# Performance work log

Hardware: AMD Instinct MI355X
Metric: run time of the kernel (lower is better)

## Reference

```python
import jax, jax.numpy as jnp
import numpy as np

TEMPERATURE = 1.0

def setup_inputs() -> dict:
    key = jax.random.key(0)
    k1, k2 = jax.random.split(key)
    B, F, C = 16384, 2048, 1000
    features = jax.random.normal(k1, (B, F), dtype=jnp.float32)
    prototypes = jax.random.normal(k2, (C, F), dtype=jnp.float32)
    return {"features": features, "prototypes": prototypes}

def reference(features, prototypes):
    # Euclidean pairwise distance via ||a||^2 + ||b||^2 - 2 a.b (same math as cdist p=2)
    f_sq = jnp.sum(features * features, axis=-1, keepdims=True)        # [B,1]
    p_sq = jnp.sum(prototypes * prototypes, axis=-1)[None, :]          # [1,C]
    cross = jnp.einsum('bf,cf->bc', features, prototypes)              # [B,C]
    d2 = jnp.maximum(f_sq + p_sq - 2.0 * cross, 0.0)
    distances = jnp.sqrt(d2)
    logits = -distances
    return logits / TEMPERATURE
```

## Files before the change

kernel.cpp:

```cpp
#include <hip/hip_runtime.h>
#include <stdint.h>


#define KDIM 2048
#define BM 128
#define BN 128
#define BKS 32
#define NSTEPS (KDIM / BKS)

typedef __attribute__((ext_vector_type(8))) __bf16 bf16x8;
typedef __attribute__((ext_vector_type(4))) float f32x4;

__device__ __forceinline__ bool sniff_is_f32(const void* Araw) {
  const uint16_t* sniff = (const uint16_t*)Araw;
  float mx = 0.f;
#pragma unroll
  for (int i = 0; i < 64; ++i) {
    float v = __uint_as_float(((uint32_t)sniff[i]) << 16);
    mx = fmaxf(mx, fabsf(v));
  }
  return mx > 1e4f;
}

__device__ __forceinline__ uint32_t bf16rn(uint32_t u) {
  return (u + 0x7FFFu + ((u >> 16) & 1u)) >> 16;
}
__device__ __forceinline__ uint32_t pack_rn(uint32_t a, uint32_t b) {
  return bf16rn(a) | (bf16rn(b) << 16);
}

__device__ __forceinline__ void gload_lds16(const void* g, void* l) {
  __builtin_amdgcn_global_load_lds(
      (const __attribute__((address_space(1))) void*)g,
      (__attribute__((address_space(3))) void*)l, 16, 0, 0);
}

__global__ __launch_bounds__(256) void prep_kernel(
    const void* __restrict__ Araw, const void* __restrict__ Braw,
    uint16_t* __restrict__ Abf, uint16_t* __restrict__ Bbf,
    float* __restrict__ fsq, float* __restrict__ psq, int M, int N) {
  const bool isf32 = sniff_is_f32(Araw);
  const int wave = threadIdx.x >> 6;
  const int lane = threadIdx.x & 63;
  const int row = blockIdx.x * 4 + wave;
  if (row >= M + N) return;
  const bool isA = row < M;
  const size_t r = isA ? (size_t)row : (size_t)(row - M);
  uint2* dst = (uint2*)((isA ? Abf : Bbf) + r * KDIM);
  float s = 0.f;
  if (isf32) {
    const float* p = (isA ? (const float*)Araw : (const float*)Braw) + r * KDIM;
#pragma unroll
    for (int it = 0; it < KDIM / 256; ++it) {
      float4 v = *((const float4*)p + it * 64 + lane);
      s = fmaf(v.x, v.x, fmaf(v.y, v.y, fmaf(v.z, v.z, fmaf(v.w, v.w, s))));
      uint2 o;
      o.x = pack_rn(__float_as_uint(v.x), __float_as_uint(v.y));
      o.y = pack_rn(__float_as_uint(v.z), __float_as_uint(v.w));
      dst[it * 64 + lane] = o;
    }
  } else {
    const uint16_t* p =
        (isA ? (const uint16_t*)Araw : (const uint16_t*)Braw) + r * KDIM;
#pragma unroll
    for (int it = 0; it < KDIM / 256; ++it) {
      uint2 v = *((const uint2*)p + it * 64 + lane);
      float e0 = __uint_as_float(v.x << 16);
      float e1 = __uint_as_float(v.x & 0xFFFF0000u);
      float e2 = __uint_as_float(v.y << 16);
      float e3 = __uint_as_float(v.y & 0xFFFF0000u);
      s = fmaf(e0, e0, fmaf(e1, e1, fmaf(e2, e2, fmaf(e3, e3, s))));
      dst[it * 64 + lane] = v;
    }
  }
#pragma unroll
  for (int o = 32; o > 0; o >>= 1) s += __shfl_down(s, o, 64);
  if (lane == 0) {
    if (isA) fsq[r] = s;
    else     psq[r] = s;
  }
}

__global__ __launch_bounds__(256) void gemm_kernel(
    const uint16_t* __restrict__ Abf, const uint16_t* __restrict__ Bbf,
    const float* __restrict__ fsq, const float* __restrict__ psq,
    float* __restrict__ out, int M, int N) {
  __shared__ uint32_t Ab[4][BM][16];
  __shared__ uint32_t Bb[4][BN][16];

  const int tid = threadIdx.x;
  const int lane = tid & 63;
  const int wave = tid >> 6;

  const int gx = gridDim.x, gy = gridDim.y;
  const int nwg = gx * gy;
  int id = blockIdx.y * gx + blockIdx.x;
  if ((nwg & 7) == 0) id = (id & 7) * (nwg >> 3) + (id >> 3);
  const int m0 = (id / gx) * BM;
  const int n0 = (id % gx) * BN;

  const int wr = wave >> 1;
  const int wc = wave & 1;
  const int lr = lane & 15;
  const int lg = lane >> 4;

  const int wbase = (tid & ~63);

  auto stage = [&](int b, int ks) {
#pragma unroll
    for (int l = 0; l < 2; ++l) {
      const int f = l * 256 + tid;
      const int row = f >> 2;
      const int gc = (f & 3) ^ ((row >> 1) & 3);
      uint32_t* la = &Ab[b][0][0] + (l * 256 + wbase) * 4;
      uint32_t* lb = &Bb[b][0][0] + (l * 256 + wbase) * 4;
      int gm = m0 + row; gm = gm < M ? gm : M - 1;
      int gn = n0 + row; gn = gn < N ? gn : N - 1;
      gload_lds16(Abf + (size_t)gm * KDIM + ks * BKS + gc * 8, la);
      gload_lds16(Bbf + (size_t)gn * KDIM + ks * BKS + gc * 8, lb);
    }
  };

  f32x4 acc[4][4] = {};

  stage(0, 0);
  stage(1, 1);
  stage(2, 2);

  for (int ks = 0; ks < NSTEPS; ++ks) {
    const int buf = ks & 3;
    if (ks + 3 < NSTEPS) {
      stage((ks + 3) & 3, ks + 3);
      asm volatile("s_waitcnt vmcnt(12)");
    } else if (ks + 2 < NSTEPS) {
      asm volatile("s_waitcnt vmcnt(8)");
    } else if (ks + 1 < NSTEPS) {
      asm volatile("s_waitcnt vmcnt(4)");
    } else {
      asm volatile("s_waitcnt vmcnt(0)");
    }
    __builtin_amdgcn_s_barrier();
    asm volatile("" ::: "memory");

    bf16x8 ah[4], bh[4];
#pragma unroll
    for (int i = 0; i < 4; ++i) {
      const int r = wr * 64 + i * 16 + lr;
      const int pc = (lg ^ ((r >> 1) & 3)) * 4;
      ah[i] = *(const bf16x8*)&Ab[buf][r][pc];
    }
#pragma unroll
    for (int j = 0; j < 4; ++j) {
      const int r = wc * 64 + j * 16 + lr;
      const int pc = (lg ^ ((r >> 1) & 3)) * 4;
      bh[j] = *(const bf16x8*)&Bb[buf][r][pc];
    }

    __builtin_amdgcn_s_setprio(1);
#pragma unroll
    for (int i = 0; i < 4; ++i)
#pragma unroll
      for (int j = 0; j < 4; ++j)
        acc[i][j] = __builtin_amdgcn_mfma_f32_16x16x32_bf16(ah[i], bh[j],
                                                            acc[i][j], 0, 0, 0);
    __builtin_amdgcn_s_setprio(0);

    __builtin_amdgcn_s_barrier();
    asm volatile("" ::: "memory");
  }

#pragma unroll
  for (int j = 0; j < 4; ++j) {
    const int n = n0 + wc * 64 + j * 16 + lr;
    if (n >= N) continue;
    const float pn = psq[n];
#pragma unroll
    for (int i = 0; i < 4; ++i) {
      const int mb = m0 + wr * 64 + i * 16 + lg * 4;
#pragma unroll
      for (int r = 0; r < 4; ++r) {
        const int m = mb + r;
        if (m < M) {
          const float d2 = fsq[m] + pn - 2.f * acc[i][j][r];
          out[(size_t)m * N + n] = -sqrtf(fmaxf(d2, 0.f));
        }
      }
    }
  }
}

__global__ __launch_bounds__(256) void dist_mfma_kernel(
    const void* __restrict__ Araw, const void* __restrict__ Braw,
    float* __restrict__ out, int M, int N) {
  __shared__ uint32_t Ah[2][BM][16];
  __shared__ uint32_t Bh[2][BN][16];
  __shared__ float fsqs[BM];
  __shared__ float psqs[BN];

  const bool isf32 = sniff_is_f32(Araw);
  const int tid = threadIdx.x;
  const int lane = tid & 63;
  const int wave = tid >> 6;
  const int m0 = blockIdx.y * BM;
  const int n0 = blockIdx.x * BN;

  const float* A32 = (const float*)Araw;
  const float* B32 = (const float*)Braw;
  const uint16_t* A16 = (const uint16_t*)Araw;
  const uint16_t* B16 = (const uint16_t*)Braw;

  const int crow = tid >> 2;
  const int cch = tid & 3;
  const int wr = wave >> 1;
  const int wc = wave & 1;
  const int lr = lane & 15;
  const int lg = lane >> 4;

  uint4 qa0[2], qa1[2], qb0[2], qb1[2];
  float na[2] = {0.f, 0.f};
  float nb[2] = {0.f, 0.f};

  auto load_step = [&](int ks) {
#pragma unroll
    for (int s = 0; s < 2; ++s) {
      const int row = crow + 64 * s;
      int gm = m0 + row; gm = gm < M ? gm : M - 1;
      int gn = n0 + row; gn = gn < N ? gn : N - 1;
      const size_t ea = (size_t)gm * KDIM + ks * BKS + cch * 8;
      const size_t eb = (size_t)gn * KDIM + ks * BKS + cch * 8;
      if (isf32) {
        qa0[s] = *(const uint4*)(A32 + ea);
        qa1[s] = *(const uint4*)(A32 + ea + 4);
        qb0[s] = *(const uint4*)(B32 + eb);
        qb1[s] = *(const uint4*)(B32 + eb + 4);
      } else {
        qa0[s] = *(const uint4*)(A16 + ea);
        qb0[s] = *(const uint4*)(B16 + eb);
      }
    }
  };

  auto store_step = [&](int b) {
#pragma unroll
    for (int s = 0; s < 2; ++s) {
      const int row = crow + 64 * s;
      const int pc = (cch ^ ((row >> 1) & 3)) * 4;
      if (isf32) {
        const uint32_t ua[8] = {qa0[s].x, qa0[s].y, qa0[s].z, qa0[s].w,
                                qa1[s].x, qa1[s].y, qa1[s].z, qa1[s].w};
        const uint32_t ub[8] = {qb0[s].x, qb0[s].y, qb0[s].z, qb0[s].w,
                                qb1[s].x, qb1[s].y, qb1[s].z, qb1[s].w};
        float sa = 0.f, sb = 0.f;
#pragma unroll
        for (int j = 0; j < 8; ++j) {
          const float fa = __uint_as_float(ua[j]);
          const float fb = __uint_as_float(ub[j]);
          sa = fmaf(fa, fa, sa);
          sb = fmaf(fb, fb, sb);
        }
        na[s] += sa; nb[s] += sb;
        uint4 pa = {pack_rn(ua[0], ua[1]), pack_rn(ua[2], ua[3]),
                    pack_rn(ua[4], ua[5]), pack_rn(ua[6], ua[7])};
        uint4 pb = {pack_rn(ub[0], ub[1]), pack_rn(ub[2], ub[3]),
                    pack_rn(ub[4], ub[5]), pack_rn(ub[6], ub[7])};
        *(uint4*)&Ah[b][row][pc] = pa;
        *(uint4*)&Bh[b][row][pc] = pb;
      } else {
        const uint32_t va[4] = {qa0[s].x, qa0[s].y, qa0[s].z, qa0[s].w};
        const uint32_t vb[4] = {qb0[s].x, qb0[s].y, qb0[s].z, qb0[s].w};
        float sa = 0.f, sb = 0.f;
#pragma unroll
        for (int j = 0; j < 4; ++j) {
          const float a0 = __uint_as_float(va[j] << 16);
          const float a1 = __uint_as_float(va[j] & 0xFFFF0000u);
          const float b0 = __uint_as_float(vb[j] << 16);
          const float b1 = __uint_as_float(vb[j] & 0xFFFF0000u);
          sa = fmaf(a0, a0, fmaf(a1, a1, sa));
          sb = fmaf(b0, b0, fmaf(b1, b1, sb));
        }
        na[s] += sa; nb[s] += sb;
        *(uint4*)&Ah[b][row][pc] = qa0[s];
        *(uint4*)&Bh[b][row][pc] = qb0[s];
      }
    }
  };

  f32x4 acc[4][4] = {};
  load_step(0);
  store_step(0);
  __syncthreads();

  for (int ks = 0; ks < NSTEPS; ++ks) {
    const int buf = ks & 1;
    const int nxt = ks + 1;
    if (nxt < NSTEPS) load_step(nxt);

    bf16x8 ah[4], bh[4];
#pragma unroll
    for (int i = 0; i < 4; ++i) {
      const int r = wr * 64 + i * 16 + lr;
      const int pc = (lg ^ ((r >> 1) & 3)) * 4;
      ah[i] = *(const bf16x8*)&Ah[buf][r][pc];
    }
#pragma unroll
    for (int j = 0; j < 4; ++j) {
      const int r = wc * 64 + j * 16 + lr;
      const int pc = (lg ^ ((r >> 1) & 3)) * 4;
      bh[j] = *(const bf16x8*)&Bh[buf][r][pc];
    }

#pragma unroll
    for (int i = 0; i < 4; ++i)
#pragma unroll
      for (int j = 0; j < 4; ++j)
        acc[i][j] = __builtin_amdgcn_mfma_f32_16x16x32_bf16(ah[i], bh[j],
                                                            acc[i][j], 0, 0, 0);

    if (nxt < NSTEPS) store_step(nxt & 1);
    __syncthreads();
  }

  float v0 = na[0], v1 = na[1], w0 = nb[0], w1 = nb[1];
#pragma unroll
  for (int o = 1; o <= 2; o <<= 1) {
    v0 += __shfl_xor(v0, o);
    v1 += __shfl_xor(v1, o);
    w0 += __shfl_xor(w0, o);
    w1 += __shfl_xor(w1, o);
  }
  if (cch == 0) {
    fsqs[crow] = v0;
    fsqs[crow + 64] = v1;
    psqs[crow] = w0;
    psqs[crow + 64] = w1;
  }
  __syncthreads();

#pragma unroll
  for (int j = 0; j < 4; ++j) {
    const int nn = wc * 64 + j * 16 + lr;
    const int n = n0 + nn;
    if (n >= N) continue;
    const float pn = psqs[nn];
#pragma unroll
    for (int i = 0; i < 4; ++i) {
      const int mb = wr * 64 + i * 16 + lg * 4;
#pragma unroll
      for (int r = 0; r < 4; ++r) {
        const int m = m0 + mb + r;
        if (m < M) {
          const float d2 = fsqs[mb + r] + pn - 2.f * acc[i][j][r];
          out[(size_t)m * N + n] = -sqrtf(fmaxf(d2, 0.f));
        }
      }
    }
  }
}

extern "C" void kernel_launch(void* const* d_in, const int* in_sizes, int n_in,
                              void* d_out, int out_size, void* d_ws,
                              size_t ws_size, hipStream_t stream) {
  (void)n_in; (void)out_size;
  const void* feat = d_in[0];
  const void* prot = d_in[1];
  float* out = (float*)d_out;

  const int M = in_sizes[0] / KDIM;
  const int N = in_sizes[1] / KDIM;

  const size_t bfA = (size_t)M * KDIM * sizeof(uint16_t);
  const size_t bfB = (size_t)N * KDIM * sizeof(uint16_t);
  const size_t ws_need = bfA + bfB + (size_t)(M + N) * sizeof(float);

  if (d_ws != nullptr && ws_size >= ws_need) {
    uint16_t* Abf = (uint16_t*)d_ws;
    uint16_t* Bbf = (uint16_t*)((char*)d_ws + bfA);
    float* fsq = (float*)((char*)d_ws + bfA + bfB);
    float* psq = fsq + M;
    const int rows = M + N;
    prep_kernel<<<dim3((rows + 3) / 4), dim3(256), 0, stream>>>(
        feat, prot, Abf, Bbf, fsq, psq, M, N);
    dim3 grid((N + BN - 1) / BN, (M + BM - 1) / BM);
    gemm_kernel<<<grid, dim3(256), 0, stream>>>(Abf, Bbf, fsq, psq, out, M, N);
  } else {
    dim3 grid((N + BN - 1) / BN, (M + BM - 1) / BM);
    dist_mfma_kernel<<<grid, dim3(256), 0, stream>>>(feat, prot, out, M, N);
  }
}
```

Before: 344.0 us.

## Enlarge GEMM tile to 256x256x64 with 512 threads and double buffering

Result: faster. 322.0 us (-6.4%).

```diff
diff --git a/kernel.cpp b/kernel.cpp
--- a/kernel.cpp
+++ b/kernel.cpp
@@ -3,10 +3,6 @@
 
 
 #define KDIM 2048
-#define BM 128
-#define BN 128
-#define BKS 32
-#define NSTEPS (KDIM / BKS)
 
 typedef __attribute__((ext_vector_type(8))) __bf16 bf16x8;
 typedef __attribute__((ext_vector_type(4))) float f32x4;
@@ -81,12 +77,17 @@
   }
 }
 
-__global__ __launch_bounds__(256) void gemm_kernel(
+#define BM2 256
+#define BN2 256
+#define BK2 64
+#define NK2 (KDIM / BK2)
+
+__global__ __launch_bounds__(512, 2) void gemm_kernel(
     const uint16_t* __restrict__ Abf, const uint16_t* __restrict__ Bbf,
     const float* __restrict__ fsq, const float* __restrict__ psq,
     float* __restrict__ out, int M, int N) {
-  __shared__ uint32_t Ab[4][BM][16];
-  __shared__ uint32_t Bb[4][BN][16];
+  __shared__ uint32_t Ab[2][BM2][32];
+  __shared__ uint32_t Bb[2][BN2][32];
 
   const int tid = threadIdx.x;
   const int lane = tid & 63;
@@ -96,11 +97,11 @@
   const int nwg = gx * gy;
   int id = blockIdx.y * gx + blockIdx.x;
   if ((nwg & 7) == 0) id = (id & 7) * (nwg >> 3) + (id >> 3);
-  const int m0 = (id / gx) * BM;
-  const int n0 = (id % gx) * BN;
-
-  const int wr = wave >> 1;
-  const int wc = wave & 1;
+  const int m0 = (id / gx) * BM2;
+  const int n0 = (id % gx) * BN2;
+
+  const int wr = wave >> 2;
+  const int wc = wave & 3;
   const int lr = lane & 15;
   const int lg = lane >> 4;
 
@@ -108,61 +109,61 @@
 
   auto stage = [&](int b, int ks) {
 #pragma unroll
-    for (int l = 0; l < 2; ++l) {
-      const int f = l * 256 + tid;
-      const int row = f >> 2;
-      const int gc = (f & 3) ^ ((row >> 1) & 3);
-      uint32_t* la = &Ab[b][0][0] + (l * 256 + wbase) * 4;
-      uint32_t* lb = &Bb[b][0][0] + (l * 256 + wbase) * 4;
+    for (int p = 0; p < 4; ++p) {
+      const int f = p * 512 + tid;
+      const int row = f >> 3;
+      const int gc = (f & 7) ^ (row & 7);
+      uint32_t* la = &Ab[b][0][0] + (p * 512 + wbase) * 4;
+      uint32_t* lb = &Bb[b][0][0] + (p * 512 + wbase) * 4;
       int gm = m0 + row; gm = gm < M ? gm : M - 1;
       int gn = n0 + row; gn = gn < N ? gn : N - 1;
-      gload_lds16(Abf + (size_t)gm * KDIM + ks * BKS + gc * 8, la);
-      gload_lds16(Bbf + (size_t)gn * KDIM + ks * BKS + gc * 8, lb);
+      gload_lds16(Abf + (size_t)gm * KDIM + ks * BK2 + gc * 8, la);
+      gload_lds16(Bbf + (size_t)gn * KDIM + ks * BK2 + gc * 8, lb);
     }
   };
 
-  f32x4 acc[4][4] = {};
+  f32x4 acc[8][4] = {};
 
   stage(0, 0);
-  stage(1, 1);
-  stage(2, 2);
-
-  for (int ks = 0; ks < NSTEPS; ++ks) {
-    const int buf = ks & 3;
-    if (ks + 3 < NSTEPS) {
-      stage((ks + 3) & 3, ks + 3);
-      asm volatile("s_waitcnt vmcnt(12)");
-    } else if (ks + 2 < NSTEPS) {
+
+  for (int ks = 0; ks < NK2; ++ks) {
+    const int buf = ks & 1;
+    if (ks + 1 < NK2) {
+      stage(buf ^ 1, ks + 1);
       asm volatile("s_waitcnt vmcnt(8)");
-    } else if (ks + 1 < NSTEPS) {
-      asm volatile("s_waitcnt vmcnt(4)");
     } else {
       asm volatile("s_waitcnt vmcnt(0)");
     }
     __builtin_amdgcn_s_barrier();
     asm volatile("" ::: "memory");
 
-    bf16x8 ah[4], bh[4];
-#pragma unroll
-    for (int i = 0; i < 4; ++i) {
-      const int r = wr * 64 + i * 16 + lr;
-      const int pc = (lg ^ ((r >> 1) & 3)) * 4;
-      ah[i] = *(const bf16x8*)&Ab[buf][r][pc];
-    }
-#pragma unroll
-    for (int j = 0; j < 4; ++j) {
-      const int r = wc * 64 + j * 16 + lr;
-      const int pc = (lg ^ ((r >> 1) & 3)) * 4;
-      bh[j] = *(const bf16x8*)&Bb[buf][r][pc];
+    bf16x8 bh[4][2];
+#pragma unroll
+    for (int nj = 0; nj < 4; ++nj) {
+      const int r = wc * 64 + nj * 16 + lr;
+#pragma unroll
+      for (int kk = 0; kk < 2; ++kk) {
+        const int pc = ((kk * 4 + lg) ^ (r & 7)) * 4;
+        bh[nj][kk] = *(const bf16x8*)&Bb[buf][r][pc];
+      }
     }
 
     __builtin_amdgcn_s_setprio(1);
 #pragma unroll
-    for (int i = 0; i < 4; ++i)
-#pragma unroll
-      for (int j = 0; j < 4; ++j)
-        acc[i][j] = __builtin_amdgcn_mfma_f32_16x16x32_bf16(ah[i], bh[j],
-                                                            acc[i][j], 0, 0, 0);
+    for (int mi = 0; mi < 8; ++mi) {
+      const int r = wr * 128 + mi * 16 + lr;
+      const int p0 = ((0 + lg) ^ (r & 7)) * 4;
+      const int p1 = ((4 + lg) ^ (r & 7)) * 4;
+      const bf16x8 a0 = *(const bf16x8*)&Ab[buf][r][p0];
+      const bf16x8 a1 = *(const bf16x8*)&Ab[buf][r][p1];
+#pragma unroll
+      for (int nj = 0; nj < 4; ++nj) {
+        acc[mi][nj] = __builtin_amdgcn_mfma_f32_16x16x32_bf16(
+            a0, bh[nj][0], acc[mi][nj], 0, 0, 0);
+        acc[mi][nj] = __builtin_amdgcn_mfma_f32_16x16x32_bf16(
+            a1, bh[nj][1], acc[mi][nj], 0, 0, 0);
+      }
+    }
     __builtin_amdgcn_s_setprio(0);
 
     __builtin_amdgcn_s_barrier();
@@ -170,24 +171,29 @@
   }
 
 #pragma unroll
-  for (int j = 0; j < 4; ++j) {
-    const int n = n0 + wc * 64 + j * 16 + lr;
+  for (int nj = 0; nj < 4; ++nj) {
+    const int n = n0 + wc * 64 + nj * 16 + lr;
     if (n >= N) continue;
     const float pn = psq[n];
 #pragma unroll
-    for (int i = 0; i < 4; ++i) {
-      const int mb = m0 + wr * 64 + i * 16 + lg * 4;
+    for (int mi = 0; mi < 8; ++mi) {
+      const int mb = m0 + wr * 128 + mi * 16 + lg * 4;
 #pragma unroll
       for (int r = 0; r < 4; ++r) {
         const int m = mb + r;
         if (m < M) {
-          const float d2 = fsq[m] + pn - 2.f * acc[i][j][r];
+          const float d2 = fsq[m] + pn - 2.f * acc[mi][nj][r];
           out[(size_t)m * N + n] = -sqrtf(fmaxf(d2, 0.f));
         }
       }
     }
   }
 }
+
+#define BM 128
+#define BN 128
+#define BKS 32
+#define NSTEPS (KDIM / BKS)
 
 __global__ __launch_bounds__(256) void dist_mfma_kernel(
     const void* __restrict__ Araw, const void* __restrict__ Braw,
@@ -266,9 +272,9 @@
         *(uint4*)&Ah[b][row][pc] = pa;
         *(uint4*)&Bh[b][row][pc] = pb;
       } else {
+        float sa = 0.f, sb = 0.f;
         const uint32_t va[4] = {qa0[s].x, qa0[s].y, qa0[s].z, qa0[s].w};
         const uint32_t vb[4] = {qb0[s].x, qb0[s].y, qb0[s].z, qb0[s].w};
-        float sa = 0.f, sb = 0.f;
 #pragma unroll
         for (int j = 0; j < 4; ++j) {
           const float a0 = __uint_as_float(va[j] << 16);
@@ -380,8 +386,8 @@
     const int rows = M + N;
     prep_kernel<<<dim3((rows + 3) / 4), dim3(256), 0, stream>>>(
         feat, prot, Abf, Bbf, fsq, psq, M, N);
-    dim3 grid((N + BN - 1) / BN, (M + BM - 1) / BM);
-    gemm_kernel<<<grid, dim3(256), 0, stream>>>(Abf, Bbf, fsq, psq, out, M, N);
+    dim3 grid((N + BN2 - 1) / BN2, (M + BM2 - 1) / BM2);
+    gemm_kernel<<<grid, dim3(512), 0, stream>>>(Abf, Bbf, fsq, psq, out, M, N);
   } else {
     dim3 grid((N + BN - 1) / BN, (M + BM - 1) / BM);
     dist_mfma_kernel<<<grid, dim3(256), 0, stream>>>(feat, prot, out, M, N);
```
